# Performance work log

Hardware: AMD Instinct MI355X
Metric: run time of the kernel (lower is better)

The kernel has to match this reference:

```python
import jax, jax.numpy as jnp
import numpy as np

K = 5          # kernel_size per dim
B = 100        # batch size (hard-coded in source)
GRID = 28
NUM_FIRST_FC = 49  # adjs[2].size(0) = 7*7


def spline_conv(x, edge_index, pseudo, W, root, bias):
    """Degree-1 open B-spline graph conv (SplineGCN).
    x: [N, Cin]; edge_index: [2, E] (src, dst); pseudo: [E, 2] in [0,1];
    W: [K*K, Cin, Cout]; root: [Cin, Cout]; bias: [Cout].
    out_i = mean_{j->i} sum_taps b_tap(u_ij) * (x_j @ W[k_tap]) + x_i @ root + bias
    """
    N = x.shape[0]
    src, dst = edge_index[0], edge_index[1]
    pos = pseudo * (K - 1)                     # open spline: scale to [0, K-1]
    kf = jnp.floor(pos)
    frac = pos - kf                            # [E, 2]
    k0 = kf.astype(jnp.int32)
    k1 = jnp.minimum(k0 + 1, K - 1)
    # Precompute x @ W[k] for all 25 kernel indices: [N, K*K, Cout]
    y = jnp.einsum('ni,kio->nko', x, W)
    fx, fy = frac[:, 0], frac[:, 1]
    taps = [
        (k0[:, 0], k0[:, 1], (1 - fx) * (1 - fy)),
        (k0[:, 0], k1[:, 1], (1 - fx) * fy),
        (k1[:, 0], k0[:, 1], fx * (1 - fy)),
        (k1[:, 0], k1[:, 1], fx * fy),
    ]
    msg = jnp.zeros((src.shape[0], W.shape[2]), dtype=x.dtype)
    for ax, ay, w in taps:
        msg = msg + w[:, None] * y[src, ax * K + ay]   # gather [E, Cout]
    agg = jax.ops.segment_sum(msg, dst, num_segments=N)
    deg = jax.ops.segment_sum(jnp.ones_like(msg[:, 0]), dst, num_segments=N)
    return agg / jnp.maximum(deg, 1.0)[:, None] + x @ root + bias


def max_pool2(x):  # x: [b, H, W, C] -> [b, H/2, W/2, C] (same math as NCHW pool)
    b, h, w, c = x.shape
    return x.reshape(b, h // 2, 2, w // 2, 2, c).max(axis=(2, 4))


def setup_inputs() -> dict:
    key = jax.random.key(0)
    ks = jax.random.split(key, 16)
    N0, N1 = B * GRID * GRID, B * (GRID // 2) * (GRID // 2)
    E0, E1 = N0 * 8, N1 * 8
    s = 0.1
    return {
        'x': jax.random.normal(ks[0], (N0, 1), dtype=jnp.float32),
        'pseudo0': jax.random.uniform(ks[1], (E0, 2), dtype=jnp.float32),
        'pseudo1': jax.random.uniform(ks[2], (E1, 2), dtype=jnp.float32),
        'W1': jax.random.normal(ks[3], (K * K, 1, 32), dtype=jnp.float32) * s,
        'root1': jax.random.normal(ks[4], (1, 32), dtype=jnp.float32) * s,
        'b1': jnp.zeros((32,), dtype=jnp.float32),
        'W2': jax.random.normal(ks[5], (K * K, 32, 64), dtype=jnp.float32) * s,
        'root2': jax.random.normal(ks[6], (32, 64), dtype=jnp.float32) * s,
        'b2': jnp.zeros((64,), dtype=jnp.float32),
        'fc1_w': jax.random.normal(ks[7], (NUM_FIRST_FC * 64, 512), dtype=jnp.float32) * 0.02,
        'fc1_b': jnp.zeros((512,), dtype=jnp.float32),
        'fc2_w': jax.random.normal(ks[8], (512, 10), dtype=jnp.float32) * 0.02,
        'fc2_b': jnp.zeros((10,), dtype=jnp.float32),
        'edge_index0': jax.random.randint(ks[9], (2, E0), 0, N0, dtype=jnp.int32),
        'edge_index1': jax.random.randint(ks[10], (2, E1), 0, N1, dtype=jnp.int32),
    }


def reference(x, pseudo0, pseudo1, W1, root1, b1, W2, root2, b2,
              fc1_w, fc1_b, fc2_w, fc2_b, edge_index0, edge_index1):
    elu = jax.nn.elu
    # conv1 on 28x28 grid graph
    h = elu(spline_conv(x, edge_index0, pseudo0, W1, root1, b1))   # [B*784, 32]
    h = h.reshape(-1, GRID, GRID, 32)                              # [B, 28, 28, 32]
    h = max_pool2(h)                                               # [B, 14, 14, 32]
    h = h.reshape(-1, 32)                                          # [B*196, 32]
    # conv2 on 14x14 grid graph
    h = elu(spline_conv(h, edge_index1, pseudo1, W2, root2, b2))   # [B*196, 64]
    # faithful replication of the source's reshapes: (B*196) rows -> (B/4, 28, 28, 64)
    h = h.reshape(-1, GRID, GRID, 64)                              # [25, 28, 28, 64]
    h = max_pool2(h)                                               # [25, 14, 14, 64]
    h = h.reshape(-1, NUM_FIRST_FC * 64)                           # [100, 3136]
    h = elu(h @ fc1_w + fc1_b)
    # F.dropout with training=False (eval) is identity
    h = elu(h @ fc2_w + fc2_b)
    return jax.nn.log_softmax(h, axis=-1)
```

## Files before the change

kernel.cpp:

```cpp
#include <hip/hip_runtime.h>
#include <hip/hip_bf16.h>

#define KK 5
constexpr int N0 = 78400;
constexpr int E0 = 627200;
constexpr int N1 = 19600;
constexpr int E1 = 156800;
constexpr int C1 = 32, C2 = 64;
constexpr int BSZ = 100;
constexpr int FC1_IN = 3136, FC1_OUT = 512;
constexpr int NKEYS = 98000;
constexpr int NCOARSE = 383;
constexpr int CAPB = 2400;
constexpr int KEXT = 832;
constexpr int ULS = 836;
constexpr int UBS = 856;
constexpr int CH2 = 192;
constexpr int CH1 = 640;

typedef __attribute__((ext_vector_type(8))) short bf16x8;
typedef __attribute__((ext_vector_type(4))) float f32x4;

__device__ __forceinline__ unsigned short f2bf(float f) {
    union { float f; unsigned u; } v; v.f = f;
    unsigned u = v.u;
    unsigned r = (u + 0x7FFF + ((u >> 16) & 1)) >> 16;
    return (unsigned short)r;
}

__device__ __forceinline__ void taps4(float px, float py,
                                      int& a00, int& a01, int& a10, int& a11,
                                      float& fx, float& fy) {
    float kfx = floorf(px), kfy = floorf(py);
    fx = px - kfx; fy = py - kfy;
    int k0x = min(max((int)kfx, 0), KK - 1);
    int k0y = min(max((int)kfy, 0), KK - 1);
    int k1x = min(k0x + 1, KK - 1), k1y = min(k0y + 1, KK - 1);
    a00 = k0x * KK + k0y; a01 = k0x * KK + k1y;
    a10 = k1x * KK + k0y; a11 = k1x * KK + k1y;
}

__global__ void coarse_bin(const int* __restrict__ ei0, const int* __restrict__ ei1,
                           int* __restrict__ gcur, int* __restrict__ pk,
                           const float* __restrict__ fc1w, const float* __restrict__ W2,
                           const float* __restrict__ root2,
                           unsigned short* __restrict__ wt1,
                           unsigned short* __restrict__ w2t) {
    __shared__ int hist[NCOARSE];
    __shared__ int gbase[NCOARSE];
    __shared__ unsigned short tile[64 * 66];
    int t = threadIdx.x;
    if (blockIdx.x >= 192) {
        int pb = blockIdx.x - 192;
        if (pb >= 392) {
            int base = (pb - 392) * 6656;
            for (int i2 = t; i2 < 6656; i2 += 512) {
                int idx = base + i2;
                int o = idx / KEXT, k = idx - o * KEXT;
                float v = (k < 800) ? W2[k * 64 + o] : root2[(k - 800) * 64 + o];
                w2t[idx] = f2bf(v);
            }
            return;
        }
        int k0 = (pb >> 3) * 64, j0 = (pb & 7) * 64;
        int jj = t & 63, ks = t >> 6;
        for (int kk = ks; kk < 64; kk += 8)
            tile[kk * 66 + jj] = f2bf(fc1w[(k0 + kk) * FC1_OUT + j0 + jj]);
        __syncthreads();
        int kk2 = t & 63, js = t >> 6;
        for (int j2 = js; j2 < 64; j2 += 8)
            wt1[(j0 + j2) * FC1_IN + k0 + kk2] = tile[kk2 * 66 + j2];
        return;
    }
    for (int i = t; i < NCOARSE; i += 512) hist[i] = 0;
    __syncthreads();
    int e0b = blockIdx.x * 4096;
    int ids[8], keys[8], rnk[8];
#pragma unroll
    for (int j = 0; j < 8; j++) {
        int e = e0b + t + j * 512;
        int gk = -1, id = 0;
        if (e < E0) { gk = ei0[E0 + e]; id = e; }
        else if (e < E0 + E1) { int el = e - E0; gk = N0 + ei1[E1 + el]; id = el; }
        ids[j] = id; keys[j] = gk;
    }
#pragma unroll
    for (int j = 0; j < 8; j++)
        if (keys[j] >= 0) rnk[j] = atomicAdd(&hist[keys[j] >> 8], 1);
    __syncthreads();
    for (int i = t; i < NCOARSE; i += 512)
        gbase[i] = hist[i] ? atomicAdd(&gcur[i], hist[i]) : 0;
    __syncthreads();
#pragma unroll
    for (int j = 0; j < 8; j++) {
        if (keys[j] >= 0) {
            int b = keys[j] >> 8;
            int p = gbase[b] + rnk[j];
            if (p < CAPB) pk[b * CAPB + p] = ids[j] | ((keys[j] & 255) << 20);
        }
    }
}

__global__ void fine_sort(const int* __restrict__ pk, const int* __restrict__ gcur,
                          int* __restrict__ idxx, int* __restrict__ off) {
    __shared__ int cl[NCOARSE];
    __shared__ int ent[CAPB];
    __shared__ int rnk[CAPB];
    __shared__ int h2[256];
    __shared__ int sc[256];
    __shared__ int redbuf[4];
    __shared__ int baseS;
    int b = blockIdx.x, t = threadIdx.x;
    for (int i2 = t; i2 < NCOARSE; i2 += 256) cl[i2] = min(gcur[i2], CAPB);
    __syncthreads();
    {
        int s = 0;
        if (t < b) s += cl[t];
        if (t + 256 < b) s += cl[t + 256];
#pragma unroll
        for (int o2 = 32; o2 > 0; o2 >>= 1) s += __shfl_down(s, o2);
        if ((t & 63) == 0) redbuf[t >> 6] = s;
        __syncthreads();
        if (t == 0) baseS = redbuf[0] + redbuf[1] + redbuf[2] + redbuf[3];
        __syncthreads();
    }
    int base = baseS;
    int cb = cl[b];
    h2[t] = 0;
    __syncthreads();
    for (int i = t; i < cb; i += 256) {
        int v = pk[b * CAPB + i];
        ent[i] = v;
        rnk[i] = atomicAdd(&h2[(v >> 20) & 255], 1);
    }
    __syncthreads();
    int v0 = h2[t];
    sc[t] = v0;
    __syncthreads();
    for (int d = 1; d < 256; d <<= 1) {
        int add = (t >= d) ? sc[t - d] : 0;
        __syncthreads();
        sc[t] += add;
        __syncthreads();
    }
    int excl = sc[t] - v0;
    __syncthreads();
    sc[t] = excl;
    __syncthreads();
    int n = (b << 8) + t;
    if (n < NKEYS) off[n] = base + excl;
    if (b == 0 && t == 0) off[NKEYS] = E0 + E1;
    for (int i = t; i < cb; i += 256) {
        int v = ent[i];
        idxx[base + sc[(v >> 20) & 255] + rnk[i]] = v & 0xFFFFF;
    }
}

__global__ __launch_bounds__(256, 4)
void conv1_pool(const int* __restrict__ idxx, const int* __restrict__ off,
                const float* __restrict__ x, const int* __restrict__ ei0,
                const float* __restrict__ ps0, const float* __restrict__ W1,
                const float* __restrict__ root, const float* __restrict__ bias,
                float* __restrict__ p1) {
    __shared__ float S4[224 * 25];
    __shared__ float Sr[56 * 25];
    __shared__ float exv[CH1], efx[CH1], efy[CH1];
    __shared__ int   emt[CH1];
    float* h1t = S4;
    int t = threadIdx.x;
    int bb = blockIdx.x;
    int n0 = bb * 56;
    int q = t & 3, nl = t >> 2;
    bool actN = nl < 56;
    int n = n0 + (actN ? nl : 0);
    float* sp = S4 + (actN ? (nl * 4 + q) : 0) * 25;
    for (int i = t; i < 224 * 25; i += 256) S4[i] = 0.f;
    int e0 = off[n0], e1 = off[n0 + 56];
    int my0 = off[n], my1 = off[n + 1];
    for (int base = e0; base < e1; base += CH1) {
        int nE = min(e1 - base, CH1);
        __syncthreads();
        for (int j = t; j < nE; j += 256) {
            int e = idxx[base + j];
            int src = ei0[e];
            int a00, a01, a10, a11; float fx, fy;
            taps4(ps0[2 * e] * (KK - 1), ps0[2 * e + 1] * (KK - 1),
                  a00, a01, a10, a11, fx, fy);
            emt[j] = a00 | (a01 << 5) | (a10 << 10) | (a11 << 15);
            efx[j] = fx; efy[j] = fy;
            exv[j] = x[src];
        }
        __syncthreads();
        if (actN) {
            int r0 = max(my0 - base, 0), r1 = min(my1 - base, nE);
            for (int p = r0 + q; p < r1; p += 4) {
                float xv = exv[p]; int m = emt[p];
                float fx = efx[p], fy = efy[p];
                float gx = 1.f - fx, gy = 1.f - fy;
                sp[m & 31]         += gx * gy * xv;
                sp[(m >> 5) & 31]  += gx * fy * xv;
                sp[(m >> 10) & 31] += fx * gy * xv;
                sp[(m >> 15) & 31] += fx * fy * xv;
            }
        }
    }
    __syncthreads();
    for (int i2 = t; i2 < 56 * 25; i2 += 256) {
        int n2 = i2 / 25, a = i2 - n2 * 25;
        Sr[i2] = S4[(n2 * 4 + 0) * 25 + a] + S4[(n2 * 4 + 1) * 25 + a] +
                 S4[(n2 * 4 + 2) * 25 + a] + S4[(n2 * 4 + 3) * 25 + a];
    }
    __syncthreads();
    {
        int o = t & 31, ng = t >> 5;
        float w1c[25];
#pragma unroll
        for (int a = 0; a < 25; a++) w1c[a] = W1[a * C1 + o];
        float ro = root[o], bo = bias[o];
        for (int j2 = 0; j2 < 7; j2++) {
            int nl2 = ng * 7 + j2;
            int n2 = n0 + nl2;
            float acc = 0.f;
#pragma unroll
            for (int a = 0; a < 25; a++) acc += Sr[nl2 * 25 + a] * w1c[a];
            float invd = 1.f / fmaxf((float)(off[n2 + 1] - off[n2]), 1.f);
            float v = acc * invd + x[n2] * ro + bo;
            h1t[nl2 * 32 + o] = v > 0.f ? v : expm1f(v);
        }
    }
    __syncthreads();
    for (int i2 = t; i2 < 448; i2 += 256) {
        int o2 = i2 & 31, pc = i2 >> 5;
        float m0 = h1t[(2 * pc) * 32 + o2],      m1 = h1t[(2 * pc + 1) * 32 + o2];
        float m2 = h1t[(28 + 2 * pc) * 32 + o2], m3 = h1t[(28 + 2 * pc + 1) * 32 + o2];
        p1[(bb * 14 + pc) * C1 + o2] = fmaxf(fmaxf(m0, m1), fmaxf(m2, m3));
    }
}

__global__ __launch_bounds__(512, 4)
void conv2_fused(const float* __restrict__ p1, const int* __restrict__ idxx,
                 const int* __restrict__ off, const int* __restrict__ ei1,
                 const float* __restrict__ ps1,
                 const unsigned short* __restrict__ w2t,
                 const float* __restrict__ b2, float* __restrict__ h2) {
    __shared__ float Ul[16 * ULS];
    __shared__ int   es[CH2];
    __shared__ int   et[CH2];
    __shared__ float efx[CH2], efy[CH2];
    unsigned short* Ub = (unsigned short*)Ul;
    int t = threadIdx.x;
    int nb = blockIdx.x * 16;
    int i = t & 31;
    int g = t >> 5;
    float* up = Ul + g * ULS;
#pragma unroll
    for (int a = 0; a < 25; a++) up[a * 32 + i] = 0.f;
    up[800 + i] = p1[(nb + g) * C1 + i];
    int e0 = off[N0 + nb], e1 = off[N0 + nb + 16];
    int my0 = off[N0 + nb + g], my1 = off[N0 + nb + g + 1];
    for (int base = e0; base < e1; base += CH2) {
        int nE = min(e1 - base, CH2);
        __syncthreads();
        for (int j = t; j < nE; j += 512) {
            int e = idxx[base + j];
            es[j] = ei1[e];
            int a00, a01, a10, a11; float fx, fy;
            taps4(ps1[2 * e] * (KK - 1), ps1[2 * e + 1] * (KK - 1),
                  a00, a01, a10, a11, fx, fy);
            et[j] = a00 | (a01 << 5) | (a10 << 10) | (a11 << 15);
            efx[j] = fx; efy[j] = fy;
        }
        __syncthreads();
        int r0 = max(my0 - base, 0);
        int r1 = min(my1 - base, nE);
        int cnt = max(r1 - r0, 0);
        int m4 = max(cnt, __shfl_xor(cnt, 32));
        for (int jj = 0; jj < m4; jj += 4) {
            bool a0 = jj < cnt, a1 = jj + 1 < cnt, a2 = jj + 2 < cnt, a3 = jj + 3 < cnt;
            int j0 = a0 ? r0 + jj     : 0;
            int j1 = a1 ? r0 + jj + 1 : 0;
            int j2 = a2 ? r0 + jj + 2 : 0;
            int j3 = a3 ? r0 + jj + 3 : 0;
            int s0 = es[j0], s1 = es[j1], s2 = es[j2], s3 = es[j3];
            int mm0 = et[j0], mm1 = et[j1], mm2 = et[j2], mm3 = et[j3];
            float fx0 = efx[j0], fy0 = efy[j0];
            float fx1 = efx[j1], fy1 = efy[j1];
            float fx2 = efx[j2], fy2 = efy[j2];
            float fx3 = efx[j3], fy3 = efy[j3];
            float x0 = p1[s0 * C1 + i];
            float x1 = p1[s1 * C1 + i];
            float x2 = p1[s2 * C1 + i];
            float x3 = p1[s3 * C1 + i];
            if (a0) {
                float gx = 1.f - fx0, gy = 1.f - fy0;
                up[(mm0 & 31) * 32 + i]         += gx * gy * x0;
                up[((mm0 >> 5) & 31) * 32 + i]  += gx * fy0 * x0;
                up[((mm0 >> 10) & 31) * 32 + i] += fx0 * gy * x0;
                up[((mm0 >> 15) & 31) * 32 + i] += fx0 * fy0 * x0;
            }
            if (a1) {
                float gx = 1.f - fx1, gy = 1.f - fy1;
                up[(mm1 & 31) * 32 + i]         += gx * gy * x1;
                up[((mm1 >> 5) & 31) * 32 + i]  += gx * fy1 * x1;
                up[((mm1 >> 10) & 31) * 32 + i] += fx1 * gy * x1;
                up[((mm1 >> 15) & 31) * 32 + i] += fx1 * fy1 * x1;
            }
            if (a2) {
                float gx = 1.f - fx2, gy = 1.f - fy2;
                up[(mm2 & 31) * 32 + i]         += gx * gy * x2;
                up[((mm2 >> 5) & 31) * 32 + i]  += gx * fy2 * x2;
                up[((mm2 >> 10) & 31) * 32 + i] += fx2 * gy * x2;
                up[((mm2 >> 15) & 31) * 32 + i] += fx2 * fy2 * x2;
            }
            if (a3) {
                float gx = 1.f - fx3, gy = 1.f - fy3;
                up[(mm3 & 31) * 32 + i]         += gx * gy * x3;
                up[((mm3 >> 5) & 31) * 32 + i]  += gx * fy3 * x3;
                up[((mm3 >> 10) & 31) * 32 + i] += fx3 * gy * x3;
                up[((mm3 >> 15) & 31) * 32 + i] += fx3 * fy3 * x3;
            }
        }
    }
    __syncthreads();
    {
        int g2 = t >> 5, i2c = t & 31;
        int dgc = off[N0 + nb + g2 + 1] - off[N0 + nb + g2];
        float invd = 1.f / fmaxf((float)dgc, 1.f);
        const float* srcp = Ul + g2 * ULS + i2c * 26;
        float rv[26];
#pragma unroll
        for (int j = 0; j < 26; j++) {
            float v = srcp[j];
            rv[j] = (i2c * 26 + j < 800) ? v * invd : v;
        }
        __syncthreads();
        unsigned* dstp = (unsigned*)(Ub + g2 * UBS + i2c * 26);
#pragma unroll
        for (int j = 0; j < 13; j++) {
            unsigned lo = f2bf(rv[2 * j]), hi = f2bf(rv[2 * j + 1]);
            dstp[j] = lo | (hi << 16);
        }
    }
    __syncthreads();
    int wv = t >> 6, lane = t & 63, quad = lane >> 4, lrow = lane & 15;
    if (wv < 4) {
        f32x4 acc = {0.f, 0.f, 0.f, 0.f};
        const unsigned short* bbase = w2t + (wv * 16 + lrow) * KEXT;
        const unsigned short* abase = Ub + lrow * UBS;
#pragma unroll
        for (int kc = 0; kc < 26; kc++) {
            bf16x8 a = *(const bf16x8*)(abase + kc * 32 + quad * 8);
            bf16x8 b = *(const bf16x8*)(bbase + kc * 32 + quad * 8);
            acc = __builtin_amdgcn_mfma_f32_16x16x32_bf16(a, b, acc, 0, 0, 0);
        }
        int o = wv * 16 + lrow;
        float bo = b2[o];
#pragma unroll
        for (int r = 0; r < 4; r++) {
            int node = quad * 4 + r;
            float v = acc[r] + bo;
            v = v > 0.f ? v : expm1f(v);
            h2[(nb + node) * C2 + o] = v;
        }
    }
}

__global__ void pool2b(const float* __restrict__ h2, unsigned short* __restrict__ p2b) {
    int idx = blockIdx.x * blockDim.x + threadIdx.x;
    if (idx >= 112 * FC1_IN) return;
    if (idx >= 100 * FC1_IN) { p2b[idx] = 0; return; }
    int o = idx & 63; int t2 = idx >> 6;
    int c = t2 % 14; int r = (t2 / 14) % 14; int b = t2 / 196;
    const float* base = h2 + (((b * 28 + 2 * r) * 28 + 2 * c) * C2 + o);
    float m = fmaxf(fmaxf(base[0], base[C2]),
                    fmaxf(base[28 * C2], base[28 * C2 + C2]));
    p2b[idx] = f2bf(m);
}

__global__ void gemm_fc1(const unsigned short* __restrict__ p2b,
                         const unsigned short* __restrict__ wt1,
                         float* __restrict__ z1p) {
    constexpr int AS = 232;
    __shared__ unsigned short as_[16 * AS];
    int t = threadIdx.x;
    int jt = blockIdx.x, mt = blockIdx.y, kz = blockIdx.z;
    int wv = t >> 6, lane = t & 63, quad = lane >> 4, lrow = lane & 15;
    int m0 = mt * 16;
    int kbase = kz * 1568;
    const unsigned short* bbase = wt1 + (jt * 64 + wv * 16 + lrow) * FC1_IN + kbase;
    f32x4 acc = {0.f, 0.f, 0.f, 0.f};
    for (int ch = 0; ch < 7; ch++) {
        __syncthreads();
        for (int slot = t; slot < 448; slot += 256) {
            int r = slot / 28, c = slot - (slot / 28) * 28;
            *(uint4*)(as_ + r * AS + c * 8) =
                *(const uint4*)(p2b + (m0 + r) * FC1_IN + kbase + ch * 224 + c * 8);
        }
        __syncthreads();
        const unsigned short* ab = as_ + lrow * AS;
        const unsigned short* bb = bbase + ch * 224;
#pragma unroll
        for (int kk = 0; kk < 7; kk++) {
            bf16x8 a = *(const bf16x8*)(ab + kk * 32 + quad * 8);
            bf16x8 b = *(const bf16x8*)(bb + kk * 32 + quad * 8);
            acc = __builtin_amdgcn_mfma_f32_16x16x32_bf16(a, b, acc, 0, 0, 0);
        }
    }
    int n = jt * 64 + wv * 16 + lrow;
#pragma unroll
    for (int r = 0; r < 4; r++) {
        int m = m0 + quad * 4 + r;
        z1p[kz * (112 * FC1_OUT) + m * FC1_OUT + n] = acc[r];
    }
}

__global__ void fc2_lsm(const float* __restrict__ z1p, const float* __restrict__ fc1b,
                        const float* __restrict__ w, const float* __restrict__ fc2b,
                        float* __restrict__ out) {
    int b = blockIdx.x;
    int t = threadIdx.x;
    int wv = t >> 6;
    int lane = t & 63;
    float acc = 0.f;
#pragma unroll
    for (int m = 0; m < 8; m++) {
        int k = lane * 8 + m;
        float xv = fc1b[k] + z1p[b * FC1_OUT + k] + z1p[112 * FC1_OUT + b * FC1_OUT + k];
        xv = xv > 0.f ? xv : expm1f(xv);
        acc += xv * w[k * 10 + wv];
    }
#pragma unroll
    for (int off = 32; off > 0; off >>= 1) acc += __shfl_down(acc, off);
    __shared__ float zs[10];
    if (lane == 0) {
        float z = acc + fc2b[wv];
        zs[wv] = z > 0.f ? z : expm1f(z);
    }
    __syncthreads();
    if (t < 10) {
        float m = -1e30f;
        for (int jj = 0; jj < 10; jj++) m = fmaxf(m, zs[jj]);
        float s = 0.f;
        for (int jj = 0; jj < 10; jj++) s += expf(zs[jj] - m);
        out[b * 10 + t] = zs[t] - m - logf(s);
    }
}

extern "C" void kernel_launch(void* const* d_in, const int* in_sizes, int n_in,
                              void* d_out, int out_size, void* d_ws, size_t ws_size,
                              hipStream_t stream) {
    const float* x     = (const float*)d_in[0];
    const float* ps0   = (const float*)d_in[1];
    const float* ps1   = (const float*)d_in[2];
    const float* W1    = (const float*)d_in[3];
    const float* root1 = (const float*)d_in[4];
    const float* b1    = (const float*)d_in[5];
    const float* W2    = (const float*)d_in[6];
    const float* root2 = (const float*)d_in[7];
    const float* b2v   = (const float*)d_in[8];
    const float* fc1w  = (const float*)d_in[9];
    const float* fc1b  = (const float*)d_in[10];
    const float* fc2w  = (const float*)d_in[11];
    const float* fc2b  = (const float*)d_in[12];
    const int*   ei0   = (const int*)d_in[13];
    const int*   ei1   = (const int*)d_in[14];

    float* ws = (float*)d_ws;
    int* gcur  = (int*)ws;
    int* off   = (int*)(ws + 384);
    int* pk    = (int*)(ws + 98388);
    int* idxx  = (int*)(ws + 1017588);
    float* p1  = ws + 1801588;
    float* h2  = ws + 2428788;
    unsigned short* p2b = (unsigned short*)(ws + 3683188);
    float* z1p = ws + 3858804;
    unsigned short* w2t = (unsigned short*)(ws + 3973492);
    unsigned short* wt1 = (unsigned short*)(ws + 4000116);

    hipMemsetAsync(gcur, 0, (size_t)NCOARSE * sizeof(int), stream);

    coarse_bin<<<592, 512, 0, stream>>>(ei0, ei1, gcur, pk, fc1w, W2, root2, wt1, w2t);
    fine_sort<<<NCOARSE, 256, 0, stream>>>(pk, gcur, idxx, off);
    conv1_pool<<<1400, 256, 0, stream>>>(idxx, off, x, ei0, ps0,
                                         W1, root1, b1, p1);
    conv2_fused<<<N1 / 16, 512, 0, stream>>>(p1, idxx, off, ei1, ps1, w2t, b2v, h2);
    pool2b<<<(112 * FC1_IN + 255) / 256, 256, 0, stream>>>(h2, p2b);
    gemm_fc1<<<dim3(8, 7, 2), 256, 0, stream>>>(p2b, wt1, z1p);
    fc2_lsm<<<BSZ, 640, 0, stream>>>(z1p, fc1b, fc2w, fc2b, (float*)d_out);
}
```

Measured before the change: 207.6 us.

## Carry src and quantized pseudo through sort; raise fc1 split-K to seven

The binning and sort kernels now carry each edge's source index and a 16-bit fixed-point pseudo coordinate pair as an int2 record. The conv kernels therefore read one contiguous record instead of doing dependent random gathers into edge_index and pseudo. This doubles the size of the sort scratch traffic and quantizes the pseudo coordinates, which can perturb the spline weights slightly. Separately, the fc1 GEMM split-K grows from 2 to 7 slices for more parallelism, and fc2 now reduces the extra partial sums.

```diff
diff --git a/kernel.cpp b/kernel.cpp
--- a/kernel.cpp
+++ b/kernel.cpp
@@ -17,6 +17,7 @@
 constexpr int UBS = 856;
 constexpr int CH2 = 192;
 constexpr int CH1 = 640;
+constexpr int KZ = 7;
 
 typedef __attribute__((ext_vector_type(8))) short bf16x8;
 typedef __attribute__((ext_vector_type(4))) float f32x4;
@@ -41,7 +42,8 @@
 }
 
 __global__ void coarse_bin(const int* __restrict__ ei0, const int* __restrict__ ei1,
-                           int* __restrict__ gcur, int* __restrict__ pk,
+                           const float* __restrict__ ps0, const float* __restrict__ ps1,
+                           int* __restrict__ gcur, int2* __restrict__ pk2,
                            const float* __restrict__ fc1w, const float* __restrict__ W2,
                            const float* __restrict__ root2,
                            unsigned short* __restrict__ wt1,
@@ -75,14 +77,26 @@
     for (int i = t; i < NCOARSE; i += 512) hist[i] = 0;
     __syncthreads();
     int e0b = blockIdx.x * 4096;
-    int ids[8], keys[8], rnk[8];
+    int keys[8], rnk[8], pay0[8], pay1[8];
 #pragma unroll
     for (int j = 0; j < 8; j++) {
         int e = e0b + t + j * 512;
-        int gk = -1, id = 0;
-        if (e < E0) { gk = ei0[E0 + e]; id = e; }
-        else if (e < E0 + E1) { int el = e - E0; gk = N0 + ei1[E1 + el]; id = el; }
-        ids[j] = id; keys[j] = gk;
+        int gk = -1, p0 = 0, p1v = 0;
+        if (e < E0) {
+            gk = ei0[E0 + e];
+            float px = ps0[2 * e] * 4.f, py = ps0[2 * e + 1] * 4.f;
+            unsigned ux = min((unsigned)(px * 16384.f + 0.5f), 65535u);
+            unsigned uy = min((unsigned)(py * 16384.f + 0.5f), 65535u);
+            p0 = ei0[e]; p1v = (int)(ux | (uy << 16));
+        } else if (e < E0 + E1) {
+            int el = e - E0;
+            gk = N0 + ei1[E1 + el];
+            float px = ps1[2 * el] * 4.f, py = ps1[2 * el + 1] * 4.f;
+            unsigned ux = min((unsigned)(px * 16384.f + 0.5f), 65535u);
+            unsigned uy = min((unsigned)(py * 16384.f + 0.5f), 65535u);
+            p0 = ei1[el]; p1v = (int)(ux | (uy << 16));
+        }
+        keys[j] = gk; pay0[j] = p0; pay1[j] = p1v;
     }
 #pragma unroll
     for (int j = 0; j < 8; j++)
@@ -96,15 +110,16 @@
         if (keys[j] >= 0) {
             int b = keys[j] >> 8;
             int p = gbase[b] + rnk[j];
-            if (p < CAPB) pk[b * CAPB + p] = ids[j] | ((keys[j] & 255) << 20);
-        }
-    }
-}
-
-__global__ void fine_sort(const int* __restrict__ pk, const int* __restrict__ gcur,
-                          int* __restrict__ idxx, int* __restrict__ off) {
+            if (p < CAPB)
+                pk2[b * CAPB + p] = make_int2(pay0[j] | ((keys[j] & 255) << 20), pay1[j]);
+        }
+    }
+}
+
+__global__ void fine_sort(const int2* __restrict__ pk2, const int* __restrict__ gcur,
+                          int2* __restrict__ erec, int* __restrict__ off) {
     __shared__ int cl[NCOARSE];
-    __shared__ int ent[CAPB];
+    __shared__ int2 ent[CAPB];
     __shared__ int rnk[CAPB];
     __shared__ int h2[256];
     __shared__ int sc[256];
@@ -129,9 +144,9 @@
     h2[t] = 0;
     __syncthreads();
     for (int i = t; i < cb; i += 256) {
-        int v = pk[b * CAPB + i];
+        int2 v = pk2[b * CAPB + i];
         ent[i] = v;
-        rnk[i] = atomicAdd(&h2[(v >> 20) & 255], 1);
+        rnk[i] = atomicAdd(&h2[(v.x >> 20) & 255], 1);
     }
     __syncthreads();
     int v0 = h2[t];
@@ -151,15 +166,15 @@
     if (n < NKEYS) off[n] = base + excl;
     if (b == 0 && t == 0) off[NKEYS] = E0 + E1;
     for (int i = t; i < cb; i += 256) {
-        int v = ent[i];
-        idxx[base + sc[(v >> 20) & 255] + rnk[i]] = v & 0xFFFFF;
+        int2 v = ent[i];
+        erec[base + sc[(v.x >> 20) & 255] + rnk[i]] = v;
     }
 }
 
 __global__ __launch_bounds__(256, 4)
-void conv1_pool(const int* __restrict__ idxx, const int* __restrict__ off,
-                const float* __restrict__ x, const int* __restrict__ ei0,
-                const float* __restrict__ ps0, const float* __restrict__ W1,
+void conv1_pool(const int2* __restrict__ erec, const int* __restrict__ off,
+                const float* __restrict__ x,
+                const float* __restrict__ W1,
                 const float* __restrict__ root, const float* __restrict__ bias,
                 float* __restrict__ p1) {
     __shared__ float S4[224 * 25];
@@ -181,11 +196,12 @@
         int nE = min(e1 - base, CH1);
         __syncthreads();
         for (int j = t; j < nE; j += 256) {
-            int e = idxx[base + j];
-            int src = ei0[e];
+            int2 r = erec[base + j];
+            int src = r.x & 0xFFFFF;
+            float px = (float)((unsigned)r.y & 0xFFFF) * (1.f / 16384.f);
+            float py = (float)((unsigned)r.y >> 16) * (1.f / 16384.f);
             int a00, a01, a10, a11; float fx, fy;
-            taps4(ps0[2 * e] * (KK - 1), ps0[2 * e + 1] * (KK - 1),
-                  a00, a01, a10, a11, fx, fy);
+            taps4(px, py, a00, a01, a10, a11, fx, fy);
             emt[j] = a00 | (a01 << 5) | (a10 << 10) | (a11 << 15);
             efx[j] = fx; efy[j] = fy;
             exv[j] = x[src];
@@ -238,9 +254,8 @@
 }
 
 __global__ __launch_bounds__(512, 4)
-void conv2_fused(const float* __restrict__ p1, const int* __restrict__ idxx,
-                 const int* __restrict__ off, const int* __restrict__ ei1,
-                 const float* __restrict__ ps1,
+void conv2_fused(const float* __restrict__ p1, const int2* __restrict__ erec,
+                 const int* __restrict__ off,
                  const unsigned short* __restrict__ w2t,
                  const float* __restrict__ b2, float* __restrict__ h2) {
     __shared__ float Ul[16 * ULS];
@@ -262,11 +277,12 @@
         int nE = min(e1 - base, CH2);
         __syncthreads();
         for (int j = t; j < nE; j += 512) {
-            int e = idxx[base + j];
-            es[j] = ei1[e];
+            int2 r = erec[base + j];
+            es[j] = r.x & 0xFFFFF;
+            float px = (float)((unsigned)r.y & 0xFFFF) * (1.f / 16384.f);
+            float py = (float)((unsigned)r.y >> 16) * (1.f / 16384.f);
             int a00, a01, a10, a11; float fx, fy;
-            taps4(ps1[2 * e] * (KK - 1), ps1[2 * e + 1] * (KK - 1),
-                  a00, a01, a10, a11, fx, fy);
+            taps4(px, py, a00, a01, a10, a11, fx, fy);
             et[j] = a00 | (a01 << 5) | (a10 << 10) | (a11 << 15);
             efx[j] = fx; efy[j] = fy;
         }
@@ -386,10 +402,10 @@
     int jt = blockIdx.x, mt = blockIdx.y, kz = blockIdx.z;
     int wv = t >> 6, lane = t & 63, quad = lane >> 4, lrow = lane & 15;
     int m0 = mt * 16;
-    int kbase = kz * 1568;
+    int kbase = kz * 448;
     const unsigned short* bbase = wt1 + (jt * 64 + wv * 16 + lrow) * FC1_IN + kbase;
     f32x4 acc = {0.f, 0.f, 0.f, 0.f};
-    for (int ch = 0; ch < 7; ch++) {
+    for (int ch = 0; ch < 2; ch++) {
         __syncthreads();
         for (int slot = t; slot < 448; slot += 256) {
             int r = slot / 28, c = slot - (slot / 28) * 28;
@@ -425,7 +441,10 @@
 #pragma unroll
     for (int m = 0; m < 8; m++) {
         int k = lane * 8 + m;
-        float xv = fc1b[k] + z1p[b * FC1_OUT + k] + z1p[112 * FC1_OUT + b * FC1_OUT + k];
+        float xv = fc1b[k];
+#pragma unroll
+        for (int p = 0; p < KZ; p++)
+            xv += z1p[p * (112 * FC1_OUT) + b * FC1_OUT + k];
         xv = xv > 0.f ? xv : expm1f(xv);
         acc += xv * w[k * 10 + wv];
     }
@@ -466,25 +485,25 @@
     const int*   ei1   = (const int*)d_in[14];
 
     float* ws = (float*)d_ws;
-    int* gcur  = (int*)ws;
-    int* off   = (int*)(ws + 384);
-    int* pk    = (int*)(ws + 98388);
-    int* idxx  = (int*)(ws + 1017588);
-    float* p1  = ws + 1801588;
-    float* h2  = ws + 2428788;
-    unsigned short* p2b = (unsigned short*)(ws + 3683188);
-    float* z1p = ws + 3858804;
-    unsigned short* w2t = (unsigned short*)(ws + 3973492);
-    unsigned short* wt1 = (unsigned short*)(ws + 4000116);
+    int*  gcur = (int*)ws;
+    int*  off  = (int*)(ws + 384);
+    int2* pk2  = (int2*)(ws + 98388);
+    int2* erec = (int2*)(ws + 1936788);
+    float* p1  = ws + 3504788;
+    float* h2  = ws + 4131988;
+    unsigned short* p2b = (unsigned short*)(ws + 5386388);
+    float* z1p = ws + 5474196;
+    unsigned short* w2t = (unsigned short*)(ws + 5875604);
+    unsigned short* wt1 = (unsigned short*)(ws + 5888916);
 
     hipMemsetAsync(gcur, 0, (size_t)NCOARSE * sizeof(int), stream);
 
-    coarse_bin<<<592, 512, 0, stream>>>(ei0, ei1, gcur, pk, fc1w, W2, root2, wt1, w2t);
-    fine_sort<<<NCOARSE, 256, 0, stream>>>(pk, gcur, idxx, off);
-    conv1_pool<<<1400, 256, 0, stream>>>(idxx, off, x, ei0, ps0,
-                                         W1, root1, b1, p1);
-    conv2_fused<<<N1 / 16, 512, 0, stream>>>(p1, idxx, off, ei1, ps1, w2t, b2v, h2);
+    coarse_bin<<<592, 512, 0, stream>>>(ei0, ei1, ps0, ps1, gcur, pk2,
+                                        fc1w, W2, root2, wt1, w2t);
+    fine_sort<<<NCOARSE, 256, 0, stream>>>(pk2, gcur, erec, off);
+    conv1_pool<<<1400, 256, 0, stream>>>(erec, off, x, W1, root1, b1, p1);
+    conv2_fused<<<N1 / 16, 512, 0, stream>>>(p1, erec, off, w2t, b2v, h2);
     pool2b<<<(112 * FC1_IN + 255) / 256, 256, 0, stream>>>(h2, p2b);
-    gemm_fc1<<<dim3(8, 7, 2), 256, 0, stream>>>(p2b, wt1, z1p);
+    gemm_fc1<<<dim3(8, 7, KZ), 256, 0, stream>>>(p2b, wt1, z1p);
     fc2_lsm<<<BSZ, 640, 0, stream>>>(z1p, fc1b, fc2w, fc2b, (float*)d_out);
 }
```

Measured after the change: 201.2 us. 3.1% less time.
